# Kernel optimization log

Hardware: AMD Instinct MI355X
Metric: run time of the kernel (lower is better)

## Reference

```python
import jax, jax.numpy as jnp
import numpy as np

N = 50000        # nodes
E = 1600000      # edges (before self loops)
IN = 128         # in_channels
HID = 32         # hidden_channels
HEADS = 4
OUT = 16         # out_channels
B = 512          # graphs in batch
NEG_SLOPE = 0.2  # PyG GATConv default


def _uniform(key, shape, fan_in):
    s = 1.0 / np.sqrt(fan_in)
    return jax.random.uniform(key, shape, jnp.float32, -s, s)


def setup_inputs() -> dict:
    key = jax.random.key(0)
    ks = jax.random.split(key, 12)
    x = jax.random.normal(ks[0], (N, IN), jnp.float32)
    edge_index = jax.random.randint(ks[1], (2, E), 0, N, dtype=jnp.int64)
    batch = jnp.sort(jax.random.randint(ks[2], (N,), 0, B, dtype=jnp.int64))
    return {
        "x": x,
        "edge_index": edge_index,
        "batch": batch,
        "W1": _uniform(ks[3], (IN, HEADS * HID), IN),
        "att_src": _uniform(ks[4], (HEADS, HID), HID),
        "att_dst": _uniform(ks[5], (HEADS, HID), HID),
        "b1": jnp.zeros((HEADS * HID,), jnp.float32),
        "lin1_w": _uniform(ks[6], (HEADS * HID, HID), HEADS * HID),
        "lin1_b": _uniform(ks[7], (HID,), HEADS * HID),
        "lin2_w": _uniform(ks[8], (HID, OUT), HID),
        "lin2_b": _uniform(ks[9], (OUT,), HID),
    }


def _gat_conv(x, src, dst, W1, att_src, att_dst, b1):
    # h: [N, H, C]
    h = (x @ W1).reshape(N, HEADS, HID)
    a_s = (h * att_src).sum(-1)   # [N, H]
    a_d = (h * att_dst).sum(-1)   # [N, H]
    # per-edge attention logits [E', H]
    alpha = jax.nn.leaky_relu(a_s[src] + a_d[dst], negative_slope=NEG_SLOPE)
    # segment softmax over incoming edges of each destination node
    amax = jax.lax.stop_gradient(jax.ops.segment_max(alpha, dst, num_segments=N))
    ex = jnp.exp(alpha - amax[dst])
    den = jax.ops.segment_sum(ex, dst, num_segments=N)
    a = ex / (den[dst] + 1e-16)
    # weighted scatter-aggregate of source features: [N, H, C]
    out = jax.ops.segment_sum(h[src] * a[:, :, None], dst, num_segments=N)
    return out.reshape(N, HEADS * HID) + b1


def reference(x, edge_index, batch, W1, att_src, att_dst, b1, lin1_w, lin1_b, lin2_w, lin2_b):
    # add self loops (PyG GATConv default add_self_loops=True)
    loop = jnp.arange(N, dtype=edge_index.dtype)
    src = jnp.concatenate([edge_index[0], loop])
    dst = jnp.concatenate([edge_index[1], loop])
    # dropout layers are identity in eval mode
    xh = jax.nn.elu(_gat_conv(x, src, dst, W1, att_src, att_dst, b1))
    g = jax.ops.segment_sum(xh, batch, num_segments=B)  # global_add_pool -> [B, H*C]
    g = g @ lin1_w + lin1_b
    return g @ lin2_w + lin2_b
```

## Files before the change

### kernel.cpp

```cpp
#include <hip/hip_runtime.h>
#include <hip/hip_bf16.h>
#include <hip/hip_fp16.h>

#define N_NODES 50000
#define E_EDGES 1600000
#define IN_CH 128
#define HID 32
#define HEADS 4
#define HC (HEADS * HID)
#define OUT_CH 16
#define B_GRAPHS 512
#define NEG_SLOPE 0.2f
#define CAP 96
#define NB 256
#define BNODES 196
#define PCAP 7168
#define ACHUNK 4096
#define APART 391
#define ROWS_PB 64
#define GEMM_BLOCKS 782
#define TOT_BLOCKS 1173

__device__ __forceinline__ unsigned short f2bf(float f) {
    unsigned int u = __float_as_uint(f);
    unsigned int r = (u + 0x7FFFu + ((u >> 16) & 1u)) >> 16;
    return (unsigned short)r;
}

__device__ __forceinline__ float lrelu_exp(float v) {
    v = v > 0.f ? v : NEG_SLOPE * v;
    return __expf(v);
}

__global__ __launch_bounds__(256) void k_fused(const float* __restrict__ x,
                                               const float* __restrict__ W1,
                                               const float* __restrict__ att_src,
                                               const float* __restrict__ att_dst,
                                               const int* __restrict__ ei,
                                               unsigned short* __restrict__ hb,
                                               float* __restrict__ a_s,
                                               float* __restrict__ a_d,
                                               int* __restrict__ gcur,
                                               unsigned int* __restrict__ ebuf,
                                               float* __restrict__ g) {
    __shared__ float smem[12288];
    const int t = threadIdx.x;
    const int bI = blockIdx.x;

    if (bI % 3 == 0) {
        const int ablk = bI / 3;
        int* scnt = (int*)smem;
        int* sbase = scnt + 4 * NB;
        const int wv = t >> 6;
        const int e0 = ablk * ACHUNK;
        int e1 = e0 + ACHUNK; if (e1 > E_EDGES) e1 = E_EDGES;
        for (int i = t; i < 4 * NB; i += 256) scnt[i] = 0;
        __syncthreads();
        const int* __restrict__ dstp = ei + E_EDGES;
        for (int e = e0 + t; e < e1; e += 256) {
            int d = dstp[e];
            atomicAdd(&scnt[wv * NB + d / BNODES], 1);
        }
        __syncthreads();
        if (t < NB) {
            int c0 = scnt[0 * NB + t], c1 = scnt[1 * NB + t];
            int c2 = scnt[2 * NB + t], c3 = scnt[3 * NB + t];
            int base = atomicAdd(&gcur[t], c0 + c1 + c2 + c3);
            sbase[0 * NB + t] = base;
            sbase[1 * NB + t] = base + c0;
            sbase[2 * NB + t] = base + c0 + c1;
            sbase[3 * NB + t] = base + c0 + c1 + c2;
            scnt[0 * NB + t] = 0; scnt[1 * NB + t] = 0;
            scnt[2 * NB + t] = 0; scnt[3 * NB + t] = 0;
        }
        __syncthreads();
        for (int e = e0 + t; e < e1; e += 256) {
            int d = dstp[e];
            int s = ei[e];
            int b = d / BNODES;
            int dl = d - b * BNODES;
            int pos = sbase[wv * NB + b] + atomicAdd(&scnt[wv * NB + b], 1);
            if (pos < PCAP)
                ebuf[(size_t)b * PCAP + pos] = ((unsigned int)dl << 16) | (unsigned int)s;
        }
        return;
    }

    float* sX = smem;
    float* sW = smem + 8192;
    const int bid = bI - bI / 3 - 1;
    const int n0 = bid * ROWS_PB;

    int gt = bid * 256 + t;
    if (gt < B_GRAPHS * HC) g[gt] = 0.f;

    for (int i = t; i < ROWS_PB * 32; i += 256) {
        int r = i >> 5, c4 = i & 31;
        int n = n0 + r;
        float4 v = (n < N_NODES) ? ((const float4*)x)[(size_t)n * 32 + c4]
                                 : make_float4(0.f, 0.f, 0.f, 0.f);
        ((float4*)sX)[i] = v;
    }

    float acc[8][4];
#pragma unroll
    for (int j = 0; j < 8; j++)
#pragma unroll
        for (int c = 0; c < 4; c++) acc[j][c] = 0.f;

    const int tx = t & 31;
    const int ty = t >> 5;

    for (int kb = 0; kb < 4; kb++) {
        __syncthreads();
        for (int i = t; i < 32 * 32; i += 256) {
            ((float4*)sW)[i] =
                ((const float4*)W1)[(size_t)(kb * 32 + (i >> 5)) * 32 + (i & 31)];
        }
        __syncthreads();
#pragma unroll
        for (int kk = 0; kk < 32; kk += 4) {
            float4 w0 = *(float4*)&sW[(kk + 0) * 128 + tx * 4];
            float4 w1 = *(float4*)&sW[(kk + 1) * 128 + tx * 4];
            float4 w2 = *(float4*)&sW[(kk + 2) * 128 + tx * 4];
            float4 w3 = *(float4*)&sW[(kk + 3) * 128 + tx * 4];
#pragma unroll
            for (int j = 0; j < 8; j++) {
                float4 xv = *(float4*)&sX[(ty * 8 + j) * 128 + kb * 32 + kk];
                acc[j][0] += xv.x * w0.x + xv.y * w1.x + xv.z * w2.x + xv.w * w3.x;
                acc[j][1] += xv.x * w0.y + xv.y * w1.y + xv.z * w2.y + xv.w * w3.y;
                acc[j][2] += xv.x * w0.z + xv.y * w1.z + xv.z * w2.z + xv.w * w3.z;
                acc[j][3] += xv.x * w0.w + xv.y * w1.w + xv.z * w2.w + xv.w * w3.w;
            }
        }
    }

#pragma unroll
    for (int j = 0; j < 8; j++) {
        int n = n0 + ty * 8 + j;
        if (n < N_NODES) {
            ushort4 o;
            o.x = f2bf(acc[j][0]); o.y = f2bf(acc[j][1]);
            o.z = f2bf(acc[j][2]); o.w = f2bf(acc[j][3]);
            *(ushort4*)&hb[(size_t)n * HC + tx * 4] = o;
        }
    }

    __syncthreads();
    float* sH = smem;
#pragma unroll
    for (int j = 0; j < 8; j++) {
        float* row = &sH[(ty * 8 + j) * 129 + tx * 4];
        row[0] = acc[j][0]; row[1] = acc[j][1];
        row[2] = acc[j][2]; row[3] = acc[j][3];
    }
    __syncthreads();
    if (t < 128) {
        int r = t & 63;
        int n = n0 + r;
        const float* __restrict__ av = (t < 64) ? att_src : att_dst;
        float s0 = 0.f, s1 = 0.f, s2 = 0.f, s3 = 0.f;
#pragma unroll 4
        for (int j = 0; j < 32; j++) {
            const float* row = &sH[r * 129 + j];
            s0 += row[0]  * av[j];
            s1 += row[32] * av[32 + j];
            s2 += row[64] * av[64 + j];
            s3 += row[96] * av[96 + j];
        }
        if (n < N_NODES) {
            float* dst = (t < 64) ? a_s : a_d;
            *(float4*)(dst + (size_t)n * 4) = make_float4(s0, s1, s2, s3);
        }
    }
}

#define NPW 13
__global__ __launch_bounds__(1024) void k_aggB(const unsigned int* __restrict__ ebuf,
                                               const int* __restrict__ gcur,
                                               const float* __restrict__ a_s,
                                               const float* __restrict__ a_d,
                                               const unsigned short* __restrict__ hb,
                                               const float* __restrict__ b1,
                                               const int* __restrict__ batch,
                                               float* __restrict__ g) {
    __shared__ unsigned short sbuf[BNODES * CAP];
    __shared__ int scnt[BNODES];
    __shared__ float sWt[16][4][97];
    const int t = threadIdx.x;
    const int b = blockIdx.x;
    const int dbase = b * BNODES;

    for (int i = t; i < BNODES; i += 1024) {
        int d = dbase + i;
        scnt[i] = (d < N_NODES) ? 1 : 0;
        sbuf[i * CAP] = (unsigned short)d;
    }
    __syncthreads();
    int m = gcur[b]; if (m > PCAP) m = PCAP;
    for (int i = t; i < m; i += 1024) {
        unsigned int p = ebuf[(size_t)b * PCAP + i];
        int dl = p >> 16;
        int s = p & 0xFFFFu;
        int c = atomicAdd(&scnt[dl], 1);
        if (c < CAP) sbuf[dl * CAP + c] = (unsigned short)s;
    }
    __syncthreads();

    const int wv = t >> 6;
    const int l = t & 63;
    const int head = l >> 4;
    const int c0 = 2 * l;
    int nl0 = wv * NPW;
    int nl1 = nl0 + NPW; if (nl1 > BNODES) nl1 = BNODES;
    int gn0 = dbase + nl0;
    if (gn0 >= N_NODES) return;
    int gn1 = dbase + nl1; if (gn1 > N_NODES) gn1 = N_NODES;
    const float2 bias = *(const float2*)(b1 + c0);
    float pool0 = 0.f, pool1 = 0.f;
    int cur = batch[gn0];
    for (int n = gn0; n < gn1; n++) {
        int bb = batch[n];
        if (bb != cur) {
            atomicAdd(&g[(size_t)cur * HC + c0], pool0);
            atomicAdd(&g[(size_t)cur * HC + c0 + 1], pool1);
            pool0 = pool1 = 0.f;
            cur = bb;
        }
        int nl = n - dbase;
        int c = scnt[nl]; if (c > CAP) c = CAP;
        float4 ad = *(const float4*)(a_d + (size_t)n * 4);
        const unsigned short* __restrict__ srow = &sbuf[nl * CAP];
        for (int i = l; i < c; i += 64) {
            int s = srow[i];
            float4 as = *(const float4*)(a_s + (size_t)s * 4);
            sWt[wv][0][i] = lrelu_exp(as.x + ad.x);
            sWt[wv][1][i] = lrelu_exp(as.y + ad.y);
            sWt[wv][2][i] = lrelu_exp(as.z + ad.z);
            sWt[wv][3][i] = lrelu_exp(as.w + ad.w);
        }
        __asm__ volatile("" ::: "memory");
        const float* __restrict__ wrow = &sWt[wv][head][0];
        float acc0 = 0.f, acc1 = 0.f, dsum = 0.f;
        int i = 0;
        for (; i + 8 <= c; i += 8) {
            unsigned int u[8];
            float w[8];
#pragma unroll
            for (int q = 0; q < 8; q++) {
                int sq = srow[i + q];
                w[q] = wrow[i + q];
                u[q] = *(const unsigned int*)(hb + (size_t)sq * HC + c0);
            }
#pragma unroll
            for (int q = 0; q < 8; q++) {
                dsum += w[q];
                acc0 += w[q] * __uint_as_float(u[q] << 16);
                acc1 += w[q] * __uint_as_float(u[q] & 0xFFFF0000u);
            }
        }
        for (; i < c; i++) {
            int s0 = srow[i];
            float w0 = wrow[i];
            unsigned int u0 = *(const unsigned int*)(hb + (size_t)s0 * HC + c0);
            dsum += w0;
            acc0 += w0 * __uint_as_float(u0 << 16);
            acc1 += w0 * __uint_as_float(u0 & 0xFFFF0000u);
        }
        __asm__ volatile("" ::: "memory");
        float inv = 1.f / (dsum + 1e-16f);
        float v0 = acc0 * inv + bias.x; v0 = v0 > 0.f ? v0 : (__expf(v0) - 1.f);
        float v1 = acc1 * inv + bias.y; v1 = v1 > 0.f ? v1 : (__expf(v1) - 1.f);
        pool0 += v0;
        pool1 += v1;
    }
    atomicAdd(&g[(size_t)cur * HC + c0], pool0);
    atomicAdd(&g[(size_t)cur * HC + c0 + 1], pool1);
}

__global__ __launch_bounds__(64) void k_mlp(const float* __restrict__ g,
                                            const float* __restrict__ w1,
                                            const float* __restrict__ bb1,
                                            const float* __restrict__ w2,
                                            const float* __restrict__ bb2,
                                            float* __restrict__ out) {
    __shared__ float sg[HC];
    __shared__ float st[HID];
    int b = blockIdx.x;
    int t = threadIdx.x;
    sg[t]      = g[(size_t)b * HC + t];
    sg[t + 64] = g[(size_t)b * HC + 64 + t];
    __syncthreads();
    if (t < HID) {
        float acc = bb1[t];
#pragma unroll 8
        for (int k = 0; k < HC; k++) acc += sg[k] * w1[(size_t)k * HID + t];
        st[t] = acc;
    }
    __syncthreads();
    if (t < OUT_CH) {
        float acc = bb2[t];
#pragma unroll
        for (int k = 0; k < HID; k++) acc += st[k] * w2[(size_t)k * OUT_CH + t];
        out[(size_t)b * OUT_CH + t] = acc;
    }
}

extern "C" void kernel_launch(void* const* d_in, const int* in_sizes, int n_in,
                              void* d_out, int out_size, void* d_ws, size_t ws_size,
                              hipStream_t stream) {
    const float* x       = (const float*)d_in[0];
    const int*   ei      = (const int*)d_in[1];
    const int*   batch   = (const int*)d_in[2];
    const float* W1      = (const float*)d_in[3];
    const float* att_src = (const float*)d_in[4];
    const float* att_dst = (const float*)d_in[5];
    const float* b1      = (const float*)d_in[6];
    const float* lin1_w  = (const float*)d_in[7];
    const float* lin1_b  = (const float*)d_in[8];
    const float* lin2_w  = (const float*)d_in[9];
    const float* lin2_b  = (const float*)d_in[10];
    float* out = (float*)d_out;

    float* ws = (float*)d_ws;
    unsigned short* hb   = (unsigned short*)ws;
    float*  a_s      = ws + 3200000;
    float*  a_d      = ws + 3400000;
    unsigned int* ebuf = (unsigned int*)(ws + 3600000);
    int*    gcur     = (int*)(ws + 5435008);
    float*  g        = ws + 5436000;

    hipMemsetAsync(gcur, 0, NB * sizeof(int), stream);

    k_fused<<<TOT_BLOCKS, 256, 0, stream>>>(
        x, W1, att_src, att_dst, ei, hb, a_s, a_d, gcur, ebuf, g);
    k_aggB<<<NB, 1024, 0, stream>>>(ebuf, gcur, a_s, a_d, hb, b1, batch, g);
    k_mlp<<<B_GRAPHS, 64, 0, stream>>>(g, lin1_w, lin1_b, lin2_w, lin2_b, out);
}
```

Baseline: 215.9 us.

## Split aggregation buckets across three blocks and fuse MLP via last-block counter

Each destination bucket is now handled by three 512-thread blocks, one per sub-range of nodes, instead of a single 1024-thread block, which should spread the aggregation over more CUs and reduce LDS per block. Attention weights are kept in fp16 in shared memory, and the GEMM K-tile is halved so the smem footprint shrinks. The separate MLP kernel is removed: the last aggregation block to finish, detected with an atomic counter, runs the two linear layers. This saves a launch but runs the MLP serially inside one block, and each sub-block rescans the whole bucket edge list.

```diff
diff --git a/kernel.cpp b/kernel.cpp
--- a/kernel.cpp
+++ b/kernel.cpp
@@ -20,6 +20,8 @@
 #define ROWS_PB 64
 #define GEMM_BLOCKS 782
 #define TOT_BLOCKS 1173
+#define AB_BLOCKS 768
+#define SUBN 66
 
 __device__ __forceinline__ unsigned short f2bf(float f) {
     unsigned int u = __float_as_uint(f);
@@ -42,8 +44,9 @@
                                                float* __restrict__ a_d,
                                                int* __restrict__ gcur,
                                                unsigned int* __restrict__ ebuf,
-                                               float* __restrict__ g) {
-    __shared__ float smem[12288];
+                                               float* __restrict__ g,
+                                               int* __restrict__ donecnt) {
+    __shared__ float smem[10240];
     const int t = threadIdx.x;
     const int bI = blockIdx.x;
 
@@ -91,6 +94,7 @@
     const int bid = bI - bI / 3 - 1;
     const int n0 = bid * ROWS_PB;
 
+    if (bid == 0 && t == 0) *donecnt = 0;
     int gt = bid * 256 + t;
     if (gt < B_GRAPHS * HC) g[gt] = 0.f;
 
@@ -111,22 +115,22 @@
     const int tx = t & 31;
     const int ty = t >> 5;
 
-    for (int kb = 0; kb < 4; kb++) {
-        __syncthreads();
-        for (int i = t; i < 32 * 32; i += 256) {
+    for (int kb = 0; kb < 8; kb++) {
+        __syncthreads();
+        for (int i = t; i < 512; i += 256) {
             ((float4*)sW)[i] =
-                ((const float4*)W1)[(size_t)(kb * 32 + (i >> 5)) * 32 + (i & 31)];
-        }
-        __syncthreads();
-#pragma unroll
-        for (int kk = 0; kk < 32; kk += 4) {
+                ((const float4*)W1)[(size_t)(kb * 16 + (i >> 5)) * 32 + (i & 31)];
+        }
+        __syncthreads();
+#pragma unroll
+        for (int kk = 0; kk < 16; kk += 4) {
             float4 w0 = *(float4*)&sW[(kk + 0) * 128 + tx * 4];
             float4 w1 = *(float4*)&sW[(kk + 1) * 128 + tx * 4];
             float4 w2 = *(float4*)&sW[(kk + 2) * 128 + tx * 4];
             float4 w3 = *(float4*)&sW[(kk + 3) * 128 + tx * 4];
 #pragma unroll
             for (int j = 0; j < 8; j++) {
-                float4 xv = *(float4*)&sX[(ty * 8 + j) * 128 + kb * 32 + kk];
+                float4 xv = *(float4*)&sX[(ty * 8 + j) * 128 + kb * 16 + kk];
                 acc[j][0] += xv.x * w0.x + xv.y * w1.x + xv.z * w2.x + xv.w * w3.x;
                 acc[j][1] += xv.x * w0.y + xv.y * w1.y + xv.z * w2.y + xv.w * w3.y;
                 acc[j][2] += xv.x * w0.z + xv.y * w1.z + xv.z * w2.z + xv.w * w3.z;
@@ -175,35 +179,47 @@
     }
 }
 
-#define NPW 13
-__global__ __launch_bounds__(1024) void k_aggB(const unsigned int* __restrict__ ebuf,
-                                               const int* __restrict__ gcur,
-                                               const float* __restrict__ a_s,
-                                               const float* __restrict__ a_d,
-                                               const unsigned short* __restrict__ hb,
-                                               const float* __restrict__ b1,
-                                               const int* __restrict__ batch,
-                                               float* __restrict__ g) {
-    __shared__ unsigned short sbuf[BNODES * CAP];
-    __shared__ int scnt[BNODES];
-    __shared__ float sWt[16][4][97];
+#define NPW 9
+__global__ __launch_bounds__(512) void k_aggB(const unsigned int* __restrict__ ebuf,
+                                              const int* __restrict__ gcur,
+                                              const float* __restrict__ a_s,
+                                              const float* __restrict__ a_d,
+                                              const unsigned short* __restrict__ hb,
+                                              const float* __restrict__ b1,
+                                              const int* __restrict__ batch,
+                                              float* __restrict__ g,
+                                              int* __restrict__ donecnt,
+                                              const float* __restrict__ w1,
+                                              const float* __restrict__ bb1,
+                                              const float* __restrict__ w2,
+                                              const float* __restrict__ bb2,
+                                              float* __restrict__ out) {
+    __shared__ unsigned short sbuf[SUBN * CAP];
+    __shared__ int scnt[SUBN];
+    __shared__ __half sWt[8][4][98];
+    __shared__ int sflag;
     const int t = threadIdx.x;
-    const int b = blockIdx.x;
-    const int dbase = b * BNODES;
-
-    for (int i = t; i < BNODES; i += 1024) {
+    const int bucket = blockIdx.x / 3;
+    const int sub = blockIdx.x % 3;
+    const int l0 = sub * SUBN;
+    const int nn = (sub == 2) ? (BNODES - 2 * SUBN) : SUBN;
+    const int dbase = bucket * BNODES + l0;
+
+    for (int i = t; i < nn; i += 512) {
         int d = dbase + i;
         scnt[i] = (d < N_NODES) ? 1 : 0;
         sbuf[i * CAP] = (unsigned short)d;
     }
     __syncthreads();
-    int m = gcur[b]; if (m > PCAP) m = PCAP;
-    for (int i = t; i < m; i += 1024) {
-        unsigned int p = ebuf[(size_t)b * PCAP + i];
-        int dl = p >> 16;
-        int s = p & 0xFFFFu;
-        int c = atomicAdd(&scnt[dl], 1);
-        if (c < CAP) sbuf[dl * CAP + c] = (unsigned short)s;
+    int m = gcur[bucket]; if (m > PCAP) m = PCAP;
+    const unsigned int* __restrict__ seg = ebuf + (size_t)bucket * PCAP;
+    for (int i = t; i < m; i += 512) {
+        unsigned int p = seg[i];
+        int dl = (int)(p >> 16) - l0;
+        if ((unsigned)dl < (unsigned)nn) {
+            int c = atomicAdd(&scnt[dl], 1);
+            if (c < CAP) sbuf[dl * CAP + c] = (unsigned short)(p & 0xFFFFu);
+        }
     }
     __syncthreads();
 
@@ -212,97 +228,100 @@
     const int head = l >> 4;
     const int c0 = 2 * l;
     int nl0 = wv * NPW;
-    int nl1 = nl0 + NPW; if (nl1 > BNODES) nl1 = BNODES;
+    int nl1 = nl0 + NPW; if (nl1 > nn) nl1 = nn;
     int gn0 = dbase + nl0;
-    if (gn0 >= N_NODES) return;
     int gn1 = dbase + nl1; if (gn1 > N_NODES) gn1 = N_NODES;
-    const float2 bias = *(const float2*)(b1 + c0);
-    float pool0 = 0.f, pool1 = 0.f;
-    int cur = batch[gn0];
-    for (int n = gn0; n < gn1; n++) {
-        int bb = batch[n];
-        if (bb != cur) {
-            atomicAdd(&g[(size_t)cur * HC + c0], pool0);
-            atomicAdd(&g[(size_t)cur * HC + c0 + 1], pool1);
-            pool0 = pool1 = 0.f;
-            cur = bb;
-        }
-        int nl = n - dbase;
-        int c = scnt[nl]; if (c > CAP) c = CAP;
-        float4 ad = *(const float4*)(a_d + (size_t)n * 4);
-        const unsigned short* __restrict__ srow = &sbuf[nl * CAP];
-        for (int i = l; i < c; i += 64) {
-            int s = srow[i];
-            float4 as = *(const float4*)(a_s + (size_t)s * 4);
-            sWt[wv][0][i] = lrelu_exp(as.x + ad.x);
-            sWt[wv][1][i] = lrelu_exp(as.y + ad.y);
-            sWt[wv][2][i] = lrelu_exp(as.z + ad.z);
-            sWt[wv][3][i] = lrelu_exp(as.w + ad.w);
-        }
-        __asm__ volatile("" ::: "memory");
-        const float* __restrict__ wrow = &sWt[wv][head][0];
-        float acc0 = 0.f, acc1 = 0.f, dsum = 0.f;
-        int i = 0;
-        for (; i + 8 <= c; i += 8) {
-            unsigned int u[8];
-            float w[8];
-#pragma unroll
-            for (int q = 0; q < 8; q++) {
-                int sq = srow[i + q];
-                w[q] = wrow[i + q];
-                u[q] = *(const unsigned int*)(hb + (size_t)sq * HC + c0);
-            }
-#pragma unroll
-            for (int q = 0; q < 8; q++) {
-                dsum += w[q];
-                acc0 += w[q] * __uint_as_float(u[q] << 16);
-                acc1 += w[q] * __uint_as_float(u[q] & 0xFFFF0000u);
-            }
-        }
-        for (; i < c; i++) {
-            int s0 = srow[i];
-            float w0 = wrow[i];
-            unsigned int u0 = *(const unsigned int*)(hb + (size_t)s0 * HC + c0);
-            dsum += w0;
-            acc0 += w0 * __uint_as_float(u0 << 16);
-            acc1 += w0 * __uint_as_float(u0 & 0xFFFF0000u);
-        }
-        __asm__ volatile("" ::: "memory");
-        float inv = 1.f / (dsum + 1e-16f);
-        float v0 = acc0 * inv + bias.x; v0 = v0 > 0.f ? v0 : (__expf(v0) - 1.f);
-        float v1 = acc1 * inv + bias.y; v1 = v1 > 0.f ? v1 : (__expf(v1) - 1.f);
-        pool0 += v0;
-        pool1 += v1;
-    }
-    atomicAdd(&g[(size_t)cur * HC + c0], pool0);
-    atomicAdd(&g[(size_t)cur * HC + c0 + 1], pool1);
-}
-
-__global__ __launch_bounds__(64) void k_mlp(const float* __restrict__ g,
-                                            const float* __restrict__ w1,
-                                            const float* __restrict__ bb1,
-                                            const float* __restrict__ w2,
-                                            const float* __restrict__ bb2,
-                                            float* __restrict__ out) {
-    __shared__ float sg[HC];
-    __shared__ float st[HID];
-    int b = blockIdx.x;
-    int t = threadIdx.x;
-    sg[t]      = g[(size_t)b * HC + t];
-    sg[t + 64] = g[(size_t)b * HC + 64 + t];
-    __syncthreads();
-    if (t < HID) {
-        float acc = bb1[t];
-#pragma unroll 8
-        for (int k = 0; k < HC; k++) acc += sg[k] * w1[(size_t)k * HID + t];
-        st[t] = acc;
-    }
-    __syncthreads();
-    if (t < OUT_CH) {
-        float acc = bb2[t];
-#pragma unroll
-        for (int k = 0; k < HID; k++) acc += st[k] * w2[(size_t)k * OUT_CH + t];
-        out[(size_t)b * OUT_CH + t] = acc;
+    if (nl0 < nn && gn0 < N_NODES) {
+        const float2 bias = *(const float2*)(b1 + c0);
+        float pool0 = 0.f, pool1 = 0.f;
+        int cur = batch[gn0];
+        for (int n = gn0; n < gn1; n++) {
+            int bb = batch[n];
+            if (bb != cur) {
+                atomicAdd(&g[(size_t)cur * HC + c0], pool0);
+                atomicAdd(&g[(size_t)cur * HC + c0 + 1], pool1);
+                pool0 = pool1 = 0.f;
+                cur = bb;
+            }
+            int nl = n - dbase;
+            int c = scnt[nl]; if (c > CAP) c = CAP;
+            float4 ad = *(const float4*)(a_d + (size_t)n * 4);
+            const unsigned short* __restrict__ srow = &sbuf[nl * CAP];
+            for (int i = l; i < c; i += 64) {
+                int s = srow[i];
+                float4 as = *(const float4*)(a_s + (size_t)s * 4);
+                sWt[wv][0][i] = __float2half(lrelu_exp(as.x + ad.x));
+                sWt[wv][1][i] = __float2half(lrelu_exp(as.y + ad.y));
+                sWt[wv][2][i] = __float2half(lrelu_exp(as.z + ad.z));
+                sWt[wv][3][i] = __float2half(lrelu_exp(as.w + ad.w));
+            }
+            __asm__ volatile("" ::: "memory");
+            const __half* __restrict__ wrow = &sWt[wv][head][0];
+            float acc0 = 0.f, acc1 = 0.f, dsum = 0.f;
+            int i = 0;
+            for (; i + 8 <= c; i += 8) {
+                unsigned int u[8];
+                float w[8];
+#pragma unroll
+                for (int q = 0; q < 8; q++) {
+                    int sq = srow[i + q];
+                    w[q] = __half2float(wrow[i + q]);
+                    u[q] = *(const unsigned int*)(hb + (size_t)sq * HC + c0);
+                }
+#pragma unroll
+                for (int q = 0; q < 8; q++) {
+                    dsum += w[q];
+                    acc0 += w[q] * __uint_as_float(u[q] << 16);
+                    acc1 += w[q] * __uint_as_float(u[q] & 0xFFFF0000u);
+                }
+            }
+            for (; i < c; i++) {
+                int s0 = srow[i];
+                float w0 = __half2float(wrow[i]);
+                unsigned int u0 = *(const unsigned int*)(hb + (size_t)s0 * HC + c0);
+                dsum += w0;
+                acc0 += w0 * __uint_as_float(u0 << 16);
+                acc1 += w0 * __uint_as_float(u0 & 0xFFFF0000u);
+            }
+            __asm__ volatile("" ::: "memory");
+            float inv = 1.f / (dsum + 1e-16f);
+            float v0 = acc0 * inv + bias.x; v0 = v0 > 0.f ? v0 : (__expf(v0) - 1.f);
+            float v1 = acc1 * inv + bias.y; v1 = v1 > 0.f ? v1 : (__expf(v1) - 1.f);
+            pool0 += v0;
+            pool1 += v1;
+        }
+        atomicAdd(&g[(size_t)cur * HC + c0], pool0);
+        atomicAdd(&g[(size_t)cur * HC + c0 + 1], pool1);
+    }
+
+    __syncthreads();
+    if (t == 0) {
+        __threadfence();
+        int old = atomicAdd(donecnt, 1);
+        sflag = (old == AB_BLOCKS - 1) ? 1 : 0;
+    }
+    __syncthreads();
+    if (sflag) {
+        __threadfence();
+        if (t < B_GRAPHS) {
+            float tacc[HID];
+#pragma unroll
+            for (int j = 0; j < HID; j++) tacc[j] = bb1[j];
+            for (int k = 0; k < HC; k++) {
+                float gv = __hip_atomic_load(&g[(size_t)t * HC + k],
+                                             __ATOMIC_RELAXED,
+                                             __HIP_MEMORY_SCOPE_AGENT);
+#pragma unroll
+                for (int j = 0; j < HID; j++) tacc[j] += gv * w1[k * HID + j];
+            }
+#pragma unroll
+            for (int o = 0; o < OUT_CH; o++) {
+                float acc = bb2[o];
+#pragma unroll
+                for (int j = 0; j < HID; j++) acc += tacc[j] * w2[j * OUT_CH + o];
+                out[(size_t)t * OUT_CH + o] = acc;
+            }
+        }
     }
 }
 
@@ -328,12 +347,14 @@
     float*  a_d      = ws + 3400000;
     unsigned int* ebuf = (unsigned int*)(ws + 3600000);
     int*    gcur     = (int*)(ws + 5435008);
+    int*    donecnt  = (int*)(ws + 5435008) + 256;
     float*  g        = ws + 5436000;
 
     hipMemsetAsync(gcur, 0, NB * sizeof(int), stream);
 
     k_fused<<<TOT_BLOCKS, 256, 0, stream>>>(
-        x, W1, att_src, att_dst, ei, hb, a_s, a_d, gcur, ebuf, g);
-    k_aggB<<<NB, 1024, 0, stream>>>(ebuf, gcur, a_s, a_d, hb, b1, batch, g);
-    k_mlp<<<B_GRAPHS, 64, 0, stream>>>(g, lin1_w, lin1_b, lin2_w, lin2_b, out);
-}
+        x, W1, att_src, att_dst, ei, hb, a_s, a_d, gcur, ebuf, g, donecnt);
+    k_aggB<<<AB_BLOCKS, 512, 0, stream>>>(
+        ebuf, gcur, a_s, a_d, hb, b1, batch, g, donecnt,
+        lin1_w, lin1_b, lin2_w, lin2_b, out);
+}
```

After: 250.3 us. 15.9% more time.
